# Kernel tuning notes

Hardware: AMD Instinct MI355X
Metric: run time of the kernel (lower is better)

The kernel has to match this reference:

```python
import jax, jax.numpy as jnp
import numpy as np

D_MODEL = 1024
N_HEADS = 16
HEAD_DIM = D_MODEL // N_HEADS
WINDOW = 256
NEG_INF = -1e30  # finite stand-in for -inf; identical softmax result, NaN-safe


def setup_inputs() -> dict:
    key = jax.random.key(0)
    ks = jax.random.split(key, 5)
    B, L = 1, 4096
    s = 1.0 / np.sqrt(D_MODEL)
    return {
        "x": jax.random.normal(ks[0], (B, L, D_MODEL), dtype=jnp.float32),
        "Wq": jax.random.normal(ks[1], (D_MODEL, D_MODEL), dtype=jnp.float32) * s,
        "Wk": jax.random.normal(ks[2], (D_MODEL, D_MODEL), dtype=jnp.float32) * s,
        "Wv": jax.random.normal(ks[3], (D_MODEL, D_MODEL), dtype=jnp.float32) * s,
        "Wo": jax.random.normal(ks[4], (D_MODEL, D_MODEL), dtype=jnp.float32) * s,
    }


def reference(x, Wq, Wk, Wv, Wo):
    B, L, _ = x.shape
    # projections (nn.Linear applies x @ W.T; weights here are stored as [out,in])
    q = (x @ Wq.T).reshape(B, L, N_HEADS, HEAD_DIM).transpose(0, 2, 1, 3)  # [B,H,L,Dh]
    k = (x @ Wk.T).reshape(B, L, N_HEADS, HEAD_DIM).transpose(0, 2, 1, 3)
    v = (x @ Wv.T).reshape(B, L, N_HEADS, HEAD_DIM).transpose(0, 2, 1, 3)

    # sliding-window causal mask: position i attends to j in [i-WINDOW+1, i]
    i = jnp.arange(L)[:, None]
    j = jnp.arange(L)[None, :]
    allowed = (j <= i) & (j >= i - WINDOW + 1)  # [L,L] bool

    scale = 1.0 / jnp.sqrt(jnp.asarray(HEAD_DIM, dtype=q.dtype))
    scores = jnp.einsum("bhqd,bhkd->bhqk", q, k) * scale  # [B,H,L,L]
    scores = jnp.where(allowed, scores, NEG_INF)
    attn = jax.nn.softmax(scores, axis=-1)
    out = jnp.einsum("bhqk,bhkd->bhqd", attn, v)  # [B,H,L,Dh]
    out = out.transpose(0, 2, 1, 3).reshape(B, L, D_MODEL)
    return out @ Wo.T
```

## Files before the change

### kernel.cpp

```cpp
#include <hip/hip_runtime.h>

using bf16x8 = __attribute__((ext_vector_type(8))) short;
using u16x8  = __attribute__((ext_vector_type(8))) unsigned short;
using f32x4  = __attribute__((ext_vector_type(4))) float;

#define LSEQ   4096
#define NH     16
#define DH     64
#define WIN    256
#define DM     1024

__device__ __forceinline__ void gl2lds16(const void* g, void* l) {
  __builtin_amdgcn_global_load_lds(
      (const __attribute__((address_space(1))) unsigned int*)g,
      (__attribute__((address_space(3))) unsigned int*)l,
      16, 0, 0);
}

__device__ __forceinline__ unsigned short f2bf(float f) {
  unsigned int u = __float_as_uint(f);
  u += 0x7fffu + ((u >> 16) & 1u);
  return (unsigned short)(u >> 16);
}

__global__ __launch_bounds__(256) void cvt_all(
    const float* __restrict__ x,  const float* __restrict__ wq,
    const float* __restrict__ wk, const float* __restrict__ wv,
    const float* __restrict__ wo, unsigned short* __restrict__ dst)
{
  const size_t i = ((size_t)blockIdx.x * 256 + threadIdx.x) * 8;
  const size_t XN = (size_t)LSEQ * DM;
  const float* src;
  size_t off;
  if (i < XN) { src = x; off = i; }
  else {
    const size_t j = i - XN;
    const int s = (int)(j >> 20);
    off = j & ((1u << 20) - 1);
    src = (s == 0) ? wq : (s == 1) ? wk : (s == 2) ? wv : wo;
  }
  const f32x4 f0 = *(const f32x4*)(src + off);
  const f32x4 f1 = *(const f32x4*)(src + off + 4);
  u16x8 o;
  o[0] = f2bf(f0[0]); o[1] = f2bf(f0[1]); o[2] = f2bf(f0[2]); o[3] = f2bf(f0[3]);
  o[4] = f2bf(f1[0]); o[5] = f2bf(f1[1]); o[6] = f2bf(f1[2]); o[7] = f2bf(f1[3]);
  *(u16x8*)(dst + i) = o;
}

__device__ __forceinline__ void gemm_tile(
    const unsigned short* __restrict__ X,
    const unsigned short* __restrict__ W,
    int m0, int n0,
    unsigned short* As, unsigned short* Bs,
    f32x4 (&acc)[4][4])
{
  const int tid  = threadIdx.x;
  const int lane = tid & 63;
  const int wave = tid >> 6;
  const int wm = wave >> 1, wn = wave & 1;
  const int fr = lane & 15, quad = lane >> 4;

  const f32x4 zero = {0.f, 0.f, 0.f, 0.f};
  #pragma unroll
  for (int i = 0; i < 4; ++i)
    #pragma unroll
    for (int j = 0; j < 4; ++j)
      acc[i][j] = zero;

  const int c0 = tid, c1 = tid + 256;
  const unsigned short* xa0 = X + (size_t)(m0 + (c0 >> 2)) * DM + (c0 & 3) * 8;
  const unsigned short* xa1 = X + (size_t)(m0 + (c1 >> 2)) * DM + (c1 & 3) * 8;
  const unsigned short* wb0 = W + (size_t)(n0 + (c0 >> 2)) * DM + (c0 & 3) * 8;
  const unsigned short* wb1 = W + (size_t)(n0 + (c1 >> 2)) * DM + (c1 & 3) * 8;
  char* la0 = (char*)As + c0 * 16;
  char* la1 = (char*)As + c1 * 16;
  char* lb0 = (char*)Bs + c0 * 16;
  char* lb1 = (char*)Bs + c1 * 16;

  for (int kt = 0; kt < DM; kt += 32) {
    gl2lds16(xa0 + kt, la0);
    gl2lds16(xa1 + kt, la1);
    gl2lds16(wb0 + kt, lb0);
    gl2lds16(wb1 + kt, lb1);
    __syncthreads();

    bf16x8 a[4], b[4];
    #pragma unroll
    for (int t = 0; t < 4; ++t)
      a[t] = *(const bf16x8*)(As + (wm * 64 + t * 16 + fr) * 32 + quad * 8);
    #pragma unroll
    for (int t = 0; t < 4; ++t)
      b[t] = *(const bf16x8*)(Bs + (wn * 64 + t * 16 + fr) * 32 + quad * 8);

    #pragma unroll
    for (int i = 0; i < 4; ++i)
      #pragma unroll
      for (int j = 0; j < 4; ++j)
        acc[i][j] = __builtin_amdgcn_mfma_f32_16x16x32_bf16(a[i], b[j], acc[i][j], 0, 0, 0);
    __syncthreads();
  }
}

__global__ __launch_bounds__(256) void proj_gemm(
    const unsigned short* __restrict__ X,
    const unsigned short* __restrict__ Wq,
    const unsigned short* __restrict__ Wk,
    const unsigned short* __restrict__ Wv,
    unsigned short* __restrict__ Qo,
    unsigned short* __restrict__ Ko,
    unsigned short* __restrict__ Vt)
{
  __shared__ unsigned short As[128 * 32];
  __shared__ unsigned short Bs[128 * 32];
  const int id = blockIdx.x;
  const int lane = threadIdx.x & 63;
  const int wave = threadIdx.x >> 6;
  const int wm = wave >> 1, wn = wave & 1;
  const int cn = lane & 15, quad = lane >> 4;
  f32x4 acc[4][4];

  if (id < 512) {
    const int m0   = (id & 31) * 128;
    const int by   = id >> 5;
    const int wsel = by >> 3;
    const int n0   = (by & 7) * 128;
    gemm_tile(X, wsel ? Wk : Wq, m0, n0, As, Bs, acc);

    const float qscl = wsel ? 1.0f : 0.180336881f;
    unsigned short* O = wsel ? Ko : Qo;
    #pragma unroll
    for (int i = 0; i < 4; ++i)
      #pragma unroll
      for (int j = 0; j < 4; ++j)
        #pragma unroll
        for (int r = 0; r < 4; ++r) {
          const int row = m0 + wm * 64 + i * 16 + quad * 4 + r;
          const int col = n0 + wn * 64 + j * 16 + cn;
          const int h = col >> 6, d = col & 63;
          O[(size_t)(h * LSEQ + row) * DH + d] = f2bf(acc[i][j][r] * qscl);
        }
  } else {
    const int vid = id - 512;
    const int m0 = (vid & 7) * 128;
    const int n0 = (vid >> 3) * 128;
    gemm_tile(Wv, X, m0, n0, As, Bs, acc);

    #pragma unroll
    for (int i = 0; i < 4; ++i)
      #pragma unroll
      for (int j = 0; j < 4; ++j)
        #pragma unroll
        for (int r = 0; r < 4; ++r) {
          const int row = m0 + wm * 64 + i * 16 + quad * 4 + r;
          const int col = n0 + wn * 64 + j * 16 + cn;
          Vt[(size_t)row * LSEQ + col] = f2bf(acc[i][j][r]);
        }
  }
}

__global__ __launch_bounds__(256) void out_gemm(
    const unsigned short* __restrict__ X,
    const unsigned short* __restrict__ W,
    float* __restrict__ O)
{
  __shared__ unsigned short As[128 * 32];
  __shared__ unsigned short Bs[128 * 32];
  const int m0 = blockIdx.x * 128;
  const int n0 = blockIdx.y * 128;
  const int lane = threadIdx.x & 63;
  const int wave = threadIdx.x >> 6;
  const int wm = wave >> 1, wn = wave & 1;
  const int cn = lane & 15, quad = lane >> 4;
  f32x4 acc[4][4];

  gemm_tile(X, W, m0, n0, As, Bs, acc);

  #pragma unroll
  for (int i = 0; i < 4; ++i)
    #pragma unroll
    for (int j = 0; j < 4; ++j)
      #pragma unroll
      for (int r = 0; r < 4; ++r) {
        const int row = m0 + wm * 64 + i * 16 + quad * 4 + r;
        const int col = n0 + wn * 64 + j * 16 + cn;
        O[(size_t)row * DM + col] = acc[i][j][r];
      }
}

#define PSTR 72
__global__ __launch_bounds__(512) void attn_fwd(
    const unsigned short* __restrict__ Q,
    const unsigned short* __restrict__ K,
    const unsigned short* __restrict__ Vt,
    unsigned short* __restrict__ Oa)
{
  __shared__ unsigned short Ks[2][64 * PSTR];
  __shared__ unsigned short Vs[2][64 * PSTR];
  __shared__ unsigned short Pl[8][16 * PSTR];
  const int id   = blockIdx.x;
  const int h    = (id & 7) | ((id >> 8) << 3);
  const int bq0  = ((id >> 3) & 31) * 128;
  const int tid  = threadIdx.x;
  const int wave = tid >> 6;
  const int lane = tid & 63;
  const int n = lane & 15, quad = lane >> 4;
  const int q0 = bq0 + wave * 16;
  unsigned short* pl = Pl[wave];

  const size_t qbase = ((size_t)(h * LSEQ + q0 + n)) * DH + quad * 8;
  const bf16x8 aq0 = *(const bf16x8*)(Q + qbase);
  const bf16x8 aq1 = *(const bf16x8*)(Q + qbase + 32);

  const int lo = (bq0 >= WIN) ? (bq0 - WIN) : 0;
  const int hi = bq0 + 128;

  const int krow = tid >> 3, part = tid & 7;
  const size_t kg = ((size_t)(h * LSEQ + krow)) * DH + part * 8;
  const size_t vg = ((size_t)(h * DH + krow)) * LSEQ + part * 8;
  const int ld = krow * PSTR + part * 8;

  {
    *(bf16x8*)(Ks[0] + ld) = *(const bf16x8*)(K  + kg + (size_t)lo * DH);
    *(bf16x8*)(Vs[0] + ld) = *(const bf16x8*)(Vt + vg + lo);
  }
  __syncthreads();

  const f32x4 zero = {0.f, 0.f, 0.f, 0.f};
  f32x4 acc[4] = {zero, zero, zero, zero};
  float li[4] = {0.f, 0.f, 0.f, 0.f};

  int t = 0;
  for (int jb = lo; jb < hi; jb += 64, ++t) {
    const int buf = t & 1;
    const bool more = (jb + 64 < hi);
    bf16x8 nk, nv;
    if (more) {
      nk = *(const bf16x8*)(K  + kg + (size_t)(jb + 64) * DH);
      nv = *(const bf16x8*)(Vt + vg + (jb + 64));
    }
    const bool active = (jb <= q0 + 15) && (jb + 63 >= q0 - (WIN - 1));
    if (active) {
      const unsigned short* ks = Ks[buf];
      const unsigned short* vs = Vs[buf];
      f32x4 s[4];
      #pragma unroll
      for (int u = 0; u < 4; ++u) {
        const bf16x8 kb0 = *(const bf16x8*)(ks + (u * 16 + n) * PSTR + quad * 8);
        const bf16x8 kb1 = *(const bf16x8*)(ks + (u * 16 + n) * PSTR + 32 + quad * 8);
        f32x4 c = zero;
        c = __builtin_amdgcn_mfma_f32_16x16x32_bf16(aq0, kb0, c, 0, 0, 0);
        c = __builtin_amdgcn_mfma_f32_16x16x32_bf16(aq1, kb1, c, 0, 0, 0);
        s[u] = c;
      }
      const bool nomask = (jb + 63 <= q0) && (jb >= q0 + 15 - (WIN - 1));
      if (nomask) {
        #pragma unroll
        for (int u = 0; u < 4; ++u)
          #pragma unroll
          for (int r = 0; r < 4; ++r) {
            const float e = __builtin_exp2f(s[u][r] - 32.0f);
            s[u][r] = e;
            li[r] += e;
          }
      } else {
        #pragma unroll
        for (int u = 0; u < 4; ++u)
          #pragma unroll
          for (int r = 0; r < 4; ++r) {
            const int qi = q0 + quad * 4 + r;
            const int kj = jb + u * 16 + n;
            const bool ok = (kj <= qi) && (kj + WIN > qi);
            const float e = __builtin_exp2f(ok ? s[u][r] - 32.0f : -1e30f);
            s[u][r] = e;
            li[r] += e;
          }
      }
      #pragma unroll
      for (int u = 0; u < 4; ++u)
        #pragma unroll
        for (int r = 0; r < 4; ++r)
          pl[(quad * 4 + r) * PSTR + u * 16 + n] = f2bf(s[u][r]);
      asm volatile("s_waitcnt lgkmcnt(0)" ::: "memory");
      const bf16x8 pa0 = *(const bf16x8*)(pl + n * PSTR + quad * 8);
      const bf16x8 pa1 = *(const bf16x8*)(pl + n * PSTR + 32 + quad * 8);
      #pragma unroll
      for (int ct = 0; ct < 4; ++ct) {
        const bf16x8 vb0 = *(const bf16x8*)(vs + (ct * 16 + n) * PSTR + quad * 8);
        const bf16x8 vb1 = *(const bf16x8*)(vs + (ct * 16 + n) * PSTR + 32 + quad * 8);
        acc[ct] = __builtin_amdgcn_mfma_f32_16x16x32_bf16(pa0, vb0, acc[ct], 0, 0, 0);
        acc[ct] = __builtin_amdgcn_mfma_f32_16x16x32_bf16(pa1, vb1, acc[ct], 0, 0, 0);
      }
    }
    if (more) {
      *(bf16x8*)(Ks[buf ^ 1] + ld) = nk;
      *(bf16x8*)(Vs[buf ^ 1] + ld) = nv;
    }
    __syncthreads();
  }

  float rd[4];
  #pragma unroll
  for (int r = 0; r < 4; ++r) {
    float v = li[r];
    v += __shfl_xor(v, 1);
    v += __shfl_xor(v, 2);
    v += __shfl_xor(v, 4);
    v += __shfl_xor(v, 8);
    rd[r] = 1.0f / v;
  }
  #pragma unroll
  for (int ct = 0; ct < 4; ++ct)
    #pragma unroll
    for (int r = 0; r < 4; ++r) {
      const int row = q0 + quad * 4 + r;
      const int col = h * DH + ct * 16 + n;
      Oa[(size_t)row * DM + col] = f2bf(acc[ct][r] * rd[r]);
    }
}

extern "C" void kernel_launch(void* const* d_in, const int* in_sizes, int n_in,
                              void* d_out, int out_size, void* d_ws, size_t ws_size,
                              hipStream_t stream) {
  const float* x  = (const float*)d_in[0];
  const float* Wq = (const float*)d_in[1];
  const float* Wk = (const float*)d_in[2];
  const float* Wv = (const float*)d_in[3];
  const float* Wo = (const float*)d_in[4];
  float* out = (float*)d_out;

  unsigned short* xb  = (unsigned short*)d_ws;
  unsigned short* Wqb = xb  + (size_t)LSEQ * DM;
  unsigned short* Wkb = Wqb + (size_t)DM * DM;
  unsigned short* Wvb = Wkb + (size_t)DM * DM;
  unsigned short* Wob = Wvb + (size_t)DM * DM;
  unsigned short* Q    = Wob + (size_t)DM * DM;
  unsigned short* K    = Q   + (size_t)LSEQ * DM;
  unsigned short* Vt   = K   + (size_t)LSEQ * DM;
  unsigned short* Attn = Vt  + (size_t)LSEQ * DM;

  cvt_all<<<dim3(4096), 256, 0, stream>>>(x, Wq, Wk, Wv, Wo, xb);
  proj_gemm<<<dim3(768), 256, 0, stream>>>(xb, Wqb, Wkb, Wvb, Q, K, Vt);
  attn_fwd<<<dim3(512), 512, 0, stream>>>(Q, K, Vt, Attn);
  out_gemm<<<dim3(32, 8), 256, 0, stream>>>(Attn, Wob, out);
}
```

Before: 160.1 us.

## Halve out_gemm M-tile to 64 rows and raise wave priority around attention MFMAs

The output projection GEMM now uses 64x128 tiles with an inline load/MFMA loop, doubling the grid from 256 to 512 blocks so more CUs are busy on the 256-CU device. In the attention kernel, s_setprio brackets the QK and PV MFMA sections so waves issuing matrix work get scheduling priority over waves doing softmax. The smaller tile cuts per-block reuse of the weight tile and adds more global traffic, and the GEMM loop is single-buffered with two barriers per k-step.

```diff
diff --git a/kernel.cpp b/kernel.cpp
--- a/kernel.cpp
+++ b/kernel.cpp
@@ -163,25 +163,61 @@
     const unsigned short* __restrict__ W,
     float* __restrict__ O)
 {
-  __shared__ unsigned short As[128 * 32];
+  __shared__ unsigned short As2[64 * 32];
   __shared__ unsigned short Bs[128 * 32];
-  const int m0 = blockIdx.x * 128;
+  const int m0 = blockIdx.x * 64;
   const int n0 = blockIdx.y * 128;
-  const int lane = threadIdx.x & 63;
-  const int wave = threadIdx.x >> 6;
+  const int tid  = threadIdx.x;
+  const int lane = tid & 63;
+  const int wave = tid >> 6;
   const int wm = wave >> 1, wn = wave & 1;
-  const int cn = lane & 15, quad = lane >> 4;
-  f32x4 acc[4][4];
-
-  gemm_tile(X, W, m0, n0, As, Bs, acc);
-
-  #pragma unroll
-  for (int i = 0; i < 4; ++i)
+  const int fr = lane & 15, quad = lane >> 4;
+
+  const f32x4 zero = {0.f, 0.f, 0.f, 0.f};
+  f32x4 acc[2][4];
+  #pragma unroll
+  for (int i = 0; i < 2; ++i)
     #pragma unroll
     for (int j = 0; j < 4; ++j)
+      acc[i][j] = zero;
+
+  const unsigned short* xa  = X + (size_t)(m0 + (tid >> 2)) * DM + (tid & 3) * 8;
+  const unsigned short* wb0 = W + (size_t)(n0 + (tid >> 2)) * DM + (tid & 3) * 8;
+  const unsigned short* wb1 = W + (size_t)(n0 + ((tid + 256) >> 2)) * DM + (tid & 3) * 8;
+  char* la  = (char*)As2 + tid * 16;
+  char* lb0 = (char*)Bs + tid * 16;
+  char* lb1 = (char*)Bs + (tid + 256) * 16;
+
+  for (int kt = 0; kt < DM; kt += 32) {
+    gl2lds16(xa + kt, la);
+    gl2lds16(wb0 + kt, lb0);
+    gl2lds16(wb1 + kt, lb1);
+    __syncthreads();
+
+    bf16x8 a[2], b[4];
+    #pragma unroll
+    for (int t = 0; t < 2; ++t)
+      a[t] = *(const bf16x8*)(As2 + (wm * 32 + t * 16 + fr) * 32 + quad * 8);
+    #pragma unroll
+    for (int t = 0; t < 4; ++t)
+      b[t] = *(const bf16x8*)(Bs + (wn * 64 + t * 16 + fr) * 32 + quad * 8);
+
+    #pragma unroll
+    for (int i = 0; i < 2; ++i)
+      #pragma unroll
+      for (int j = 0; j < 4; ++j)
+        acc[i][j] = __builtin_amdgcn_mfma_f32_16x16x32_bf16(a[i], b[j], acc[i][j], 0, 0, 0);
+    __syncthreads();
+  }
+
+  const int cn = lane & 15;
+  #pragma unroll
+  for (int i = 0; i < 2; ++i)
+    #pragma unroll
+    for (int j = 0; j < 4; ++j)
       #pragma unroll
       for (int r = 0; r < 4; ++r) {
-        const int row = m0 + wm * 64 + i * 16 + quad * 4 + r;
+        const int row = m0 + wm * 32 + i * 16 + quad * 4 + r;
         const int col = n0 + wn * 64 + j * 16 + cn;
         O[(size_t)row * DM + col] = acc[i][j][r];
       }
@@ -243,6 +279,7 @@
       const unsigned short* ks = Ks[buf];
       const unsigned short* vs = Vs[buf];
       f32x4 s[4];
+      __builtin_amdgcn_s_setprio(1);
       #pragma unroll
       for (int u = 0; u < 4; ++u) {
         const bf16x8 kb0 = *(const bf16x8*)(ks + (u * 16 + n) * PSTR + quad * 8);
@@ -252,6 +289,7 @@
         c = __builtin_amdgcn_mfma_f32_16x16x32_bf16(aq1, kb1, c, 0, 0, 0);
         s[u] = c;
       }
+      __builtin_amdgcn_s_setprio(0);
       const bool nomask = (jb + 63 <= q0) && (jb >= q0 + 15 - (WIN - 1));
       if (nomask) {
         #pragma unroll
@@ -283,6 +321,7 @@
       asm volatile("s_waitcnt lgkmcnt(0)" ::: "memory");
       const bf16x8 pa0 = *(const bf16x8*)(pl + n * PSTR + quad * 8);
       const bf16x8 pa1 = *(const bf16x8*)(pl + n * PSTR + 32 + quad * 8);
+      __builtin_amdgcn_s_setprio(1);
       #pragma unroll
       for (int ct = 0; ct < 4; ++ct) {
         const bf16x8 vb0 = *(const bf16x8*)(vs + (ct * 16 + n) * PSTR + quad * 8);
@@ -290,6 +329,7 @@
         acc[ct] = __builtin_amdgcn_mfma_f32_16x16x32_bf16(pa0, vb0, acc[ct], 0, 0, 0);
         acc[ct] = __builtin_amdgcn_mfma_f32_16x16x32_bf16(pa1, vb1, acc[ct], 0, 0, 0);
       }
+      __builtin_amdgcn_s_setprio(0);
     }
     if (more) {
       *(bf16x8*)(Ks[buf ^ 1] + ld) = nk;
@@ -341,5 +381,5 @@
   cvt_all<<<dim3(4096), 256, 0, stream>>>(x, Wq, Wk, Wv, Wo, xb);
   proj_gemm<<<dim3(768), 256, 0, stream>>>(xb, Wqb, Wkb, Wvb, Q, K, Vt);
   attn_fwd<<<dim3(512), 512, 0, stream>>>(Q, K, Vt, Attn);
-  out_gemm<<<dim3(32, 8), 256, 0, stream>>>(Attn, Wob, out);
-}
+  out_gemm<<<dim3(64, 8), 256, 0, stream>>>(Attn, Wob, out);
+}
```

After: 153.6 us. 4.0% less time.
